# Performance work log

Measured on AMD Instinct MI355X. Metric: run time of the kernel, lower is better.

Reference implementation:

```python
import jax, jax.numpy as jnp
import numpy as np

N_NODES = 50000
N_EDGES = 800000
DIM = 128
N_LAYERS = 3
N_GRAPHS = 64
NEG_SLOPE = 0.2


def setup_inputs() -> dict:
    key = jax.random.key(0)
    ks = jax.random.split(key, 9)
    x = jax.random.normal(ks[0], (N_NODES, DIM), dtype=jnp.float32)
    edge_index = jax.random.randint(ks[1], (2, N_EDGES), 0, N_NODES, dtype=jnp.int32)
    batch = jnp.sort(jax.random.randint(ks[2], (N_NODES,), 0, N_GRAPHS, dtype=jnp.int32))
    Ws = jax.random.normal(ks[3], (N_LAYERS, DIM, DIM), dtype=jnp.float32) / np.sqrt(DIM)
    att_src = jax.random.normal(ks[4], (N_LAYERS, DIM), dtype=jnp.float32) * 0.1
    att_dst = jax.random.normal(ks[5], (N_LAYERS, DIM), dtype=jnp.float32) * 0.1
    biases = jnp.zeros((N_LAYERS, DIM), dtype=jnp.float32)
    Wf = jax.random.normal(ks[6], (DIM, 1), dtype=jnp.float32) / np.sqrt(DIM)
    bf = jnp.zeros((1,), dtype=jnp.float32)
    return {"x": x, "edge_index": edge_index, "batch": batch, "Ws": Ws,
            "att_src": att_src, "att_dst": att_dst, "biases": biases,
            "Wf": Wf, "bf": bf}


def _gat_layer(x, src, dst, W, a_src, a_dst, b, n_nodes):
    # PyG GATConv, heads=1: linear transform, per-edge attention, softmax over
    # edges incoming to each dst node, scatter-add aggregation, bias.
    h = x @ W                                        # [N, H]
    alpha = jax.nn.leaky_relu(
        (h * a_src).sum(-1)[src] + (h * a_dst).sum(-1)[dst], NEG_SLOPE)  # [E]
    m = jax.ops.segment_max(alpha, dst, num_segments=n_nodes)
    e = jnp.exp(alpha - m[dst])
    s = jax.ops.segment_sum(e, dst, num_segments=n_nodes)
    w = e / (s[dst] + 1e-16)                         # softmax per dst-neighborhood
    out = jax.ops.segment_sum(w[:, None] * h[src], dst, num_segments=n_nodes)
    return out + b


def reference(x, edge_index, batch, Ws, att_src, att_dst, biases, Wf, bf):
    n_nodes = x.shape[0]
    loop = jnp.arange(n_nodes, dtype=edge_index.dtype)   # add_self_loops=True
    src = jnp.concatenate([edge_index[0], loop])
    dst = jnp.concatenate([edge_index[1], loop])
    for l in range(N_LAYERS):
        x = _gat_layer(x, src, dst, Ws[l], att_src[l], att_dst[l], biases[l], n_nodes)
        x = jax.nn.relu(x)
    pooled = jax.ops.segment_sum(x, batch, num_segments=N_GRAPHS)  # global_add_pool
    y = (pooled @ Wf + bf).squeeze(-1)               # [N_GRAPHS]
    return y
```

## Files before the change

kernel.cpp:

```cpp
#include <hip/hip_runtime.h>
#include <hip/hip_bf16.h>

#define N_NODES 50000
#define DIM 128
#define N_GRAPHS 64
#define E_RAW 800000
#define E_TOT 850000
#define E_CAP 1200000
#define NEG_SLOPE 0.2f

typedef unsigned int uint;
typedef unsigned short ushort;
typedef float v2f __attribute__((ext_vector_type(2)));
typedef short bf16x8 __attribute__((ext_vector_type(8)));
typedef float f32x4 __attribute__((ext_vector_type(4)));

__device__ __forceinline__ int pi_pos(int p) {
    return (p >> 3) + 32 * ((p >> 1) & 3) + 16 * (p & 1);
}

__device__ __forceinline__ ushort f2bf(float f) {
    uint u = __float_as_uint(f);
    u += 0x7fffu + ((u >> 16) & 1u);
    return (ushort)(u >> 16);
}

__global__ void init_kernel(int* deg, int* fillc, float* pooled) {
    int i = blockIdx.x * blockDim.x + threadIdx.x;
    if (i < N_NODES) { deg[i] = 0; fillc[i] = 0; }
    if (i < N_GRAPHS * DIM) pooled[i] = 0.f;
}

__global__ void x2bf_kernel(const float* __restrict__ x, ushort* __restrict__ xb) {
    int i = blockIdx.x * blockDim.x + threadIdx.x;
    if (i >= N_NODES * DIM / 4) return;
    float4 v = ((const float4*)x)[i];
    ushort4 o;
    o.x = f2bf(v.x); o.y = f2bf(v.y); o.z = f2bf(v.z); o.w = f2bf(v.w);
    ((ushort4*)xb)[i] = o;
}

__global__ void wprep_kernel(const float* __restrict__ Ws, ushort* __restrict__ Wfrag) {
    int t = blockIdx.x * blockDim.x + threadIdx.x;
    if (t >= 3 * 32 * 64) return;
    int l = t >> 11;
    int rem = t & 2047;
    int chunk = rem >> 6, lane = rem & 63;
    int ks = chunk >> 3, nt = chunk & 7;
    int cc = lane & 15, gg = lane >> 4;
    const float* W = Ws + (size_t)l * DIM * DIM;
    ushort o[8];
#pragma unroll
    for (int j = 0; j < 8; ++j) {
        int kp = ks * 32 + gg * 8 + j;
        int kl = (l == 0) ? kp : pi_pos(kp);
        o[j] = f2bf(W[kl * DIM + nt * 16 + cc]);
    }
#pragma unroll
    for (int j = 0; j < 8; ++j) Wfrag[(size_t)t * 8 + j] = o[j];
}

__global__ void count_kernel(const int* __restrict__ ei, int* __restrict__ deg) {
    int e = blockIdx.x * blockDim.x + threadIdx.x;
    if (e >= E_TOT) return;
    int dst = (e < E_RAW) ? ei[E_RAW + e] : (e - E_RAW);
    atomicAdd(&deg[dst], 1);
}

__global__ void scan1_kernel(const int* __restrict__ deg, int* __restrict__ excl,
                             int* __restrict__ blksum, int n) {
    __shared__ int lds[256];
    int t = threadIdx.x;
    int i = blockIdx.x * 256 + t;
    int v = (i < n) ? ((deg[i] + 3) & ~3) : 0;
    lds[t] = v;
    __syncthreads();
    int incl = v;
    for (int off = 1; off < 256; off <<= 1) {
        int y = (t >= off) ? lds[t - off] : 0;
        __syncthreads();
        incl += y;
        lds[t] = incl;
        __syncthreads();
    }
    if (i < n) excl[i] = incl - v;
    if (t == 255) blksum[blockIdx.x] = incl;
}

__global__ void scan2_kernel(int* __restrict__ blksum, int* __restrict__ row_ptr, int nblk) {
    __shared__ int lds[256];
    int t = threadIdx.x;
    int v = (t < nblk) ? blksum[t] : 0;
    lds[t] = v;
    __syncthreads();
    int incl = v;
    for (int off = 1; off < 256; off <<= 1) {
        int y = (t >= off) ? lds[t - off] : 0;
        __syncthreads();
        incl += y;
        lds[t] = incl;
        __syncthreads();
    }
    if (t < nblk) blksum[t] = incl - v;
    if (t == nblk - 1) row_ptr[N_NODES] = incl;
}

__global__ void scan3_kernel(int* __restrict__ row_ptr, const int* __restrict__ blksum, int n) {
    int i = blockIdx.x * blockDim.x + threadIdx.x;
    if (i < n) row_ptr[i] += blksum[i >> 8];
}

__global__ void pad_kernel(const int* __restrict__ deg, const int* __restrict__ row_ptr,
                           int* __restrict__ csr_src) {
    int i = blockIdx.x * blockDim.x + threadIdx.x;
    if (i >= N_NODES) return;
    int d = deg[i];
    int pd = (d + 3) & ~3;
    int base = row_ptr[i];
    for (int k = d; k < pd; ++k) csr_src[base + k] = -1;
}

__global__ void fill_kernel(const int* __restrict__ ei, const int* __restrict__ row_ptr,
                            int* __restrict__ fillc, int* __restrict__ csr_src) {
    int e = blockIdx.x * blockDim.x + threadIdx.x;
    if (e >= E_TOT) return;
    int src, dst;
    if (e < E_RAW) { src = ei[e]; dst = ei[E_RAW + e]; }
    else           { src = dst = e - E_RAW; }
    int slot = row_ptr[dst] + atomicAdd(&fillc[dst], 1);
    csr_src[slot] = src;
}

__global__ __launch_bounds__(256) void gemm_mfma_kernel(
    const ushort* __restrict__ Xb, const ushort* __restrict__ Wfrag,
    const float* __restrict__ asrc, const float* __restrict__ adst,
    uint* __restrict__ Hb, float* __restrict__ s1, float* __restrict__ s2, int nrows) {
    int wv = threadIdx.x >> 6;
    int lane = threadIdx.x & 63;
    int c = lane & 15, g = lane >> 4;
    int row0 = blockIdx.x * 64 + wv * 16;

    int arow = row0 + c;
    if (arow >= nrows) arow = nrows - 1;
    const ushort* xrow = Xb + (size_t)arow * DIM;

    f32x4 acc[8];
#pragma unroll
    for (int nt = 0; nt < 8; ++nt) acc[nt] = (f32x4)(0.f);

#pragma unroll
    for (int ks = 0; ks < 4; ++ks) {
        bf16x8 afrag = *(const bf16x8*)(xrow + ks * 32 + g * 8);
#pragma unroll
        for (int nt = 0; nt < 8; ++nt) {
            bf16x8 bfrag = *(const bf16x8*)(Wfrag + ((size_t)(ks * 8 + nt) * 64 + lane) * 8);
            acc[nt] = __builtin_amdgcn_mfma_f32_16x16x32_bf16(afrag, bfrag, acc[nt], 0, 0, 0);
        }
    }

    float a1[8], a2[8];
#pragma unroll
    for (int nt = 0; nt < 8; ++nt) { a1[nt] = asrc[c + 16 * nt]; a2[nt] = adst[c + 16 * nt]; }

#pragma unroll
    for (int r = 0; r < 4; ++r) {
        int outrow = row0 + g * 4 + r;
        bool valid = outrow < nrows;
        if (valid) {
            int w0 = __builtin_amdgcn_cvt_pk_fp8_f32(acc[0][r], acc[1][r], 0, false);
            w0     = __builtin_amdgcn_cvt_pk_fp8_f32(acc[2][r], acc[3][r], w0, true);
            int w1 = __builtin_amdgcn_cvt_pk_fp8_f32(acc[4][r], acc[5][r], 0, false);
            w1     = __builtin_amdgcn_cvt_pk_fp8_f32(acc[6][r], acc[7][r], w1, true);
            *(uint2*)&Hb[(size_t)outrow * 32 + c * 2] = make_uint2((uint)w0, (uint)w1);
        }
        float p1 = 0.f, p2 = 0.f;
#pragma unroll
        for (int nt = 0; nt < 8; ++nt) {
            p1 = fmaf(acc[nt][r], a1[nt], p1);
            p2 = fmaf(acc[nt][r], a2[nt], p2);
        }
#pragma unroll
        for (int m = 1; m < 16; m <<= 1) { p1 += __shfl_xor(p1, m); p2 += __shfl_xor(p2, m); }
        if (c == 0 && valid) { s1[outrow] = p1; s2[outrow] = p2; }
    }
}

__global__ __launch_bounds__(256) void agg_kernel(
    const ushort* __restrict__ Hb16, const int* __restrict__ csr_src,
    const int* __restrict__ row_ptr, const float* __restrict__ s1,
    const float* __restrict__ s2n, const float* __restrict__ bias,
    ushort* __restrict__ Xout, const int* __restrict__ batch,
    float* __restrict__ pooled, int pool_flag, int ngroups) {
    int gw = (blockIdx.x * blockDim.x + threadIdx.x) >> 6;
    int lane = threadIdx.x & 63;
    if (gw >= ngroups) return;
    int node0 = gw * 8;

    int4 rpa = *(const int4*)&row_ptr[node0];
    int4 rpb = *(const int4*)&row_ptr[node0 + 4];
    int rp8 = row_ptr[node0 + 8];
    int rp[9] = {rpa.x, rpa.y, rpa.z, rpa.w, rpb.x, rpb.y, rpb.z, rpb.w, rp8};
    float4 s2qa = *(const float4*)&s2n[node0];
    float4 s2qb = *(const float4*)&s2n[node0 + 4];
    float s2a[8] = {s2qa.x, s2qa.y, s2qa.z, s2qa.w, s2qb.x, s2qb.y, s2qb.z, s2qb.w};
    int cc = lane >> 2, ii = lane & 3;
    float2 b2;
    b2.x = bias[cc + 32 * ii];
    b2.y = bias[cc + 32 * ii + 16];
    int ba[8] = {0, 0, 0, 0, 0, 0, 0, 0};
    if (pool_flag) {
        int4 bqa = *(const int4*)&batch[node0];
        int4 bqb = *(const int4*)&batch[node0 + 4];
        ba[0] = bqa.x; ba[1] = bqa.y; ba[2] = bqa.z; ba[3] = bqa.w;
        ba[4] = bqb.x; ba[5] = bqb.y; ba[6] = bqb.z; ba[7] = bqb.w;
    }

#pragma unroll
    for (int k = 0; k < 8; ++k) {
        int beg = rp[k], end = rp[k + 1];
        float s2v = s2a[k];
        float2 acc = make_float2(0.f, 0.f);
        float wsum = 0.f;

        for (int s = beg; s < end; s += 8) {
            int4 a = *(const int4*)&csr_src[s];
            bool vb = (s + 4) < end;
            int4 b = vb ? *(const int4*)&csr_src[s + 4] : make_int4(-1, -1, -1, -1);
            int sn[8] = {a.x, a.y, a.z, a.w, b.x, b.y, b.z, b.w};
            ushort hv[8];
#pragma unroll
            for (int j = 0; j < 8; ++j) {
                int r = (sn[j] < 0) ? 0 : sn[j];
                hv[j] = Hb16[(size_t)r * 64 + lane];
            }
            float w[8];
#pragma unroll
            for (int j = 0; j < 8; ++j) {
                int r = (sn[j] < 0) ? 0 : sn[j];
                float al = s1[r] + s2v;
                al = (al > 0.f) ? al : NEG_SLOPE * al;
                float e = __expf(al);
                w[j] = (sn[j] < 0) ? 0.f : e;
                wsum += w[j];
            }
#pragma unroll
            for (int j = 0; j < 8; ++j) {
                v2f f = __builtin_amdgcn_cvt_pk_f32_fp8((int)hv[j], false);
                acc.x = fmaf(w[j], f.x, acc.x);
                acc.y = fmaf(w[j], f.y, acc.y);
            }
        }

        float inv = 1.f / (wsum + 1e-16f);
        acc.x = fmaxf(fmaf(acc.x, inv, b2.x), 0.f);
        acc.y = fmaxf(fmaf(acc.y, inv, b2.y), 0.f);
        if (pool_flag) {
            atomicAdd(&pooled[ba[k] * DIM + 2 * lane], acc.x);
            atomicAdd(&pooled[ba[k] * DIM + 2 * lane + 1], acc.y);
        } else {
            ushort2 hb;
            hb.x = f2bf(acc.x);
            hb.y = f2bf(acc.y);
            ((ushort2*)Xout)[(size_t)(node0 + k) * 64 + lane] = hb;
        }
    }
}

__global__ void final_kernel(const float* __restrict__ pooled, const float* __restrict__ Wf,
                             const float* __restrict__ bf, float* __restrict__ y) {
    int wid = (blockIdx.x * blockDim.x + threadIdx.x) >> 6;
    int lane = threadIdx.x & 63;
    if (wid >= N_GRAPHS) return;
    float2 p = *(const float2*)&pooled[wid * DIM + 2 * lane];
    int cc = lane >> 2, ii = lane & 3;
    float wx = Wf[cc + 32 * ii];
    float wy = Wf[cc + 32 * ii + 16];
    float v = p.x * wx + p.y * wy;
    for (int off = 32; off; off >>= 1) v += __shfl_down(v, off);
    if (lane == 0) y[wid] = v + bf[0];
}

extern "C" void kernel_launch(void* const* d_in, const int* in_sizes, int n_in,
                              void* d_out, int out_size, void* d_ws, size_t ws_size,
                              hipStream_t stream) {
    const float* x       = (const float*)d_in[0];
    const int*   ei      = (const int*)d_in[1];
    const int*   batch   = (const int*)d_in[2];
    const float* Ws      = (const float*)d_in[3];
    const float* att_src = (const float*)d_in[4];
    const float* att_dst = (const float*)d_in[5];
    const float* biases  = (const float*)d_in[6];
    const float* Wf      = (const float*)d_in[7];
    const float* bf      = (const float*)d_in[8];
    float* y = (float*)d_out;

    char* p = (char*)d_ws;
    auto alloc = [&](size_t bytes) -> void* {
        void* r = (void*)p;
        p += (bytes + 255) & ~(size_t)255;
        return r;
    };
    ushort* xC     = (ushort*)alloc((size_t)(N_NODES + 64) * DIM * 2);
    ushort* xA     = (ushort*)alloc((size_t)(N_NODES + 64) * DIM * 2);
    uint*   Hb     = (uint*)alloc((size_t)N_NODES * 32 * 4);
    ushort* Wfrag  = (ushort*)alloc((size_t)3 * 32 * 64 * 8 * 2);
    int*   csr_src = (int*)alloc((size_t)E_CAP * 4);
    int*   deg     = (int*)alloc((size_t)N_NODES * 4);
    int*   fillc   = (int*)alloc((size_t)N_NODES * 4);
    int*   row_ptr = (int*)alloc((size_t)(N_NODES + 16) * 4);
    int*   blksum  = (int*)alloc(256 * 4);
    float* s1      = (float*)alloc((size_t)N_NODES * 4);
    float* s2      = (float*)alloc((size_t)(N_NODES + 8) * 4);
    float* pooled  = (float*)alloc((size_t)N_GRAPHS * DIM * 4);

    const int BN = 256;
    const int gN   = (N_NODES + BN - 1) / BN;
    const int gE   = (E_TOT + BN - 1) / BN;
    const int ngroups = N_NODES / 8;
    const int gAGG = (ngroups * 64 + BN - 1) / BN;
    const int nblk = gN;
    const int gCVT = (N_NODES * DIM / 4 + BN - 1) / BN;
    const int gGEMM = (N_NODES + 63) / 64;

    init_kernel<<<gN, BN, 0, stream>>>(deg, fillc, pooled);
    x2bf_kernel<<<gCVT, BN, 0, stream>>>(x, xC);
    wprep_kernel<<<(3 * 32 * 64 + BN - 1) / BN, BN, 0, stream>>>(Ws, Wfrag);
    count_kernel<<<gE, BN, 0, stream>>>(ei, deg);
    scan1_kernel<<<nblk, BN, 0, stream>>>(deg, row_ptr, blksum, N_NODES);
    scan2_kernel<<<1, BN, 0, stream>>>(blksum, row_ptr, nblk);
    scan3_kernel<<<gN, BN, 0, stream>>>(row_ptr, blksum, N_NODES);
    pad_kernel<<<gN, BN, 0, stream>>>(deg, row_ptr, csr_src);
    fill_kernel<<<gE, BN, 0, stream>>>(ei, row_ptr, fillc, csr_src);

    const ushort* xin = xC;
    ushort* xout = xA;
    for (int l = 0; l < 3; ++l) {
        const ushort* Wf_l = Wfrag + (size_t)l * 32 * 64 * 8;
        const float* as = att_src + (size_t)l * DIM;
        const float* ad = att_dst + (size_t)l * DIM;
        const float* b  = biases + (size_t)l * DIM;

        gemm_mfma_kernel<<<gGEMM, BN, 0, stream>>>(xin, Wf_l, as, ad, Hb, s1, s2, N_NODES);
        agg_kernel<<<gAGG, BN, 0, stream>>>((const ushort*)Hb, csr_src, row_ptr, s1, s2, b,
                                            xout, batch, pooled,
                                            (l == 2) ? 1 : 0, ngroups);
        xin = xout;
        xout = (l == 0) ? xC : xA;
    }

    final_kernel<<<(N_GRAPHS * 64 + BN - 1) / BN, BN, 0, stream>>>(pooled, Wf, bf, y);
    (void)ws_size; (void)n_in; (void)in_sizes; (void)out_size;
}
```

Baseline: 378.1 us.

## Precompute per-edge attention weights in a separate kernel and split gather across half-waves

Adds an ew_kernel that computes the leaky-relu/exp attention weight for every CSR slot once per layer, using a new csr_dst array written during fill. The aggregation kernel then loads precomputed weights instead of gathering s1 and evaluating exp redundantly in all 64 lanes. Each half-wave now gathers a different neighbour as a 4-byte fp8 word and the halves are combined with a shuffle. Padding is replaced by pre-filling csr_src with -1 over a fixed slot count. The cost is an extra kernel launch and extra weight and dst traffic each layer, and correctness depends on padded slots staying within NSLOT.

```diff
diff --git a/kernel.cpp b/kernel.cpp
--- a/kernel.cpp
+++ b/kernel.cpp
@@ -6,6 +6,7 @@
 #define N_GRAPHS 64
 #define E_RAW 800000
 #define E_TOT 850000
+#define NSLOT 1000000
 #define E_CAP 1200000
 #define NEG_SLOPE 0.2f
 
@@ -29,6 +30,11 @@
     int i = blockIdx.x * blockDim.x + threadIdx.x;
     if (i < N_NODES) { deg[i] = 0; fillc[i] = 0; }
     if (i < N_GRAPHS * DIM) pooled[i] = 0.f;
+}
+
+__global__ void csr_init_kernel(int* __restrict__ csr_src) {
+    int i = blockIdx.x * blockDim.x + threadIdx.x;
+    if (i < NSLOT / 4) ((int4*)csr_src)[i] = make_int4(-1, -1, -1, -1);
 }
 
 __global__ void x2bf_kernel(const float* __restrict__ x, ushort* __restrict__ xb) {
@@ -110,18 +116,9 @@
     if (i < n) row_ptr[i] += blksum[i >> 8];
 }
 
-__global__ void pad_kernel(const int* __restrict__ deg, const int* __restrict__ row_ptr,
-                           int* __restrict__ csr_src) {
-    int i = blockIdx.x * blockDim.x + threadIdx.x;
-    if (i >= N_NODES) return;
-    int d = deg[i];
-    int pd = (d + 3) & ~3;
-    int base = row_ptr[i];
-    for (int k = d; k < pd; ++k) csr_src[base + k] = -1;
-}
-
 __global__ void fill_kernel(const int* __restrict__ ei, const int* __restrict__ row_ptr,
-                            int* __restrict__ fillc, int* __restrict__ csr_src) {
+                            int* __restrict__ fillc, int* __restrict__ csr_src,
+                            int* __restrict__ csr_dst) {
     int e = blockIdx.x * blockDim.x + threadIdx.x;
     if (e >= E_TOT) return;
     int src, dst;
@@ -129,6 +126,7 @@
     else           { src = dst = e - E_RAW; }
     int slot = row_ptr[dst] + atomicAdd(&fillc[dst], 1);
     csr_src[slot] = src;
+    csr_dst[slot] = dst;
 }
 
 __global__ __launch_bounds__(256) void gemm_mfma_kernel(
@@ -185,28 +183,46 @@
     }
 }
 
+__global__ __launch_bounds__(256) void ew_kernel(
+    const int* __restrict__ csr_src, const int* __restrict__ csr_dst,
+    const float* __restrict__ s1, const float* __restrict__ s2,
+    float* __restrict__ w) {
+    int slot = blockIdx.x * blockDim.x + threadIdx.x;
+    if (slot >= NSLOT) return;
+    int sv = csr_src[slot];
+    float wv = 0.f;
+    if (sv >= 0) {
+        int dv = csr_dst[slot];
+        float al = s1[sv] + s2[dv];
+        al = fmaxf(al, NEG_SLOPE * al);
+        wv = __expf(al);
+    }
+    w[slot] = wv;
+}
+
 __global__ __launch_bounds__(256) void agg_kernel(
-    const ushort* __restrict__ Hb16, const int* __restrict__ csr_src,
-    const int* __restrict__ row_ptr, const float* __restrict__ s1,
-    const float* __restrict__ s2n, const float* __restrict__ bias,
+    const uint* __restrict__ Hb, const int* __restrict__ csr_src,
+    const int* __restrict__ row_ptr, const float* __restrict__ w,
+    const float* __restrict__ bias,
     ushort* __restrict__ Xout, const int* __restrict__ batch,
     float* __restrict__ pooled, int pool_flag, int ngroups) {
     int gw = (blockIdx.x * blockDim.x + threadIdx.x) >> 6;
     int lane = threadIdx.x & 63;
     if (gw >= ngroups) return;
     int node0 = gw * 8;
+    int q = lane & 31;
+    int h = lane >> 5;
 
     int4 rpa = *(const int4*)&row_ptr[node0];
     int4 rpb = *(const int4*)&row_ptr[node0 + 4];
     int rp8 = row_ptr[node0 + 8];
     int rp[9] = {rpa.x, rpa.y, rpa.z, rpa.w, rpb.x, rpb.y, rpb.z, rpb.w, rp8};
-    float4 s2qa = *(const float4*)&s2n[node0];
-    float4 s2qb = *(const float4*)&s2n[node0 + 4];
-    float s2a[8] = {s2qa.x, s2qa.y, s2qa.z, s2qa.w, s2qb.x, s2qb.y, s2qb.z, s2qb.w};
-    int cc = lane >> 2, ii = lane & 3;
+
+    int p0 = 4 * q + 2 * h;
     float2 b2;
-    b2.x = bias[cc + 32 * ii];
-    b2.y = bias[cc + 32 * ii + 16];
+    b2.x = bias[pi_pos(p0)];
+    b2.y = bias[pi_pos(p0) + 16];
+
     int ba[8] = {0, 0, 0, 0, 0, 0, 0, 0};
     if (pool_flag) {
         int4 bqa = *(const int4*)&batch[node0];
@@ -218,50 +234,52 @@
 #pragma unroll
     for (int k = 0; k < 8; ++k) {
         int beg = rp[k], end = rp[k + 1];
-        float s2v = s2a[k];
-        float2 acc = make_float2(0.f, 0.f);
-        float wsum = 0.f;
+        float acc0 = 0.f, acc1 = 0.f, acc2 = 0.f, acc3 = 0.f, ws = 0.f;
 
         for (int s = beg; s < end; s += 8) {
             int4 a = *(const int4*)&csr_src[s];
+            float4 wa = *(const float4*)&w[s];
             bool vb = (s + 4) < end;
             int4 b = vb ? *(const int4*)&csr_src[s + 4] : make_int4(-1, -1, -1, -1);
+            float4 wb = vb ? *(const float4*)&w[s + 4] : make_float4(0.f, 0.f, 0.f, 0.f);
             int sn[8] = {a.x, a.y, a.z, a.w, b.x, b.y, b.z, b.w};
-            ushort hv[8];
-#pragma unroll
-            for (int j = 0; j < 8; ++j) {
-                int r = (sn[j] < 0) ? 0 : sn[j];
-                hv[j] = Hb16[(size_t)r * 64 + lane];
+            float wv[8] = {wa.x, wa.y, wa.z, wa.w, wb.x, wb.y, wb.z, wb.w};
+#pragma unroll
+            for (int p2 = 0; p2 < 4; ++p2) {
+                int r0 = sn[2 * p2];     r0 = (r0 < 0) ? 0 : r0;
+                int r1 = sn[2 * p2 + 1]; r1 = (r1 < 0) ? 0 : r1;
+                int rsel = h ? r1 : r0;
+                float wsel = h ? wv[2 * p2 + 1] : wv[2 * p2];
+                uint hv = Hb[(size_t)rsel * 32 + q];
+                v2f f0 = __builtin_amdgcn_cvt_pk_f32_fp8((int)hv, false);
+                v2f f1 = __builtin_amdgcn_cvt_pk_f32_fp8((int)hv, true);
+                acc0 = fmaf(wsel, f0.x, acc0);
+                acc1 = fmaf(wsel, f0.y, acc1);
+                acc2 = fmaf(wsel, f1.x, acc2);
+                acc3 = fmaf(wsel, f1.y, acc3);
+                ws += wsel;
             }
-            float w[8];
-#pragma unroll
-            for (int j = 0; j < 8; ++j) {
-                int r = (sn[j] < 0) ? 0 : sn[j];
-                float al = s1[r] + s2v;
-                al = (al > 0.f) ? al : NEG_SLOPE * al;
-                float e = __expf(al);
-                w[j] = (sn[j] < 0) ? 0.f : e;
-                wsum += w[j];
-            }
-#pragma unroll
-            for (int j = 0; j < 8; ++j) {
-                v2f f = __builtin_amdgcn_cvt_pk_f32_fp8((int)hv[j], false);
-                acc.x = fmaf(w[j], f.x, acc.x);
-                acc.y = fmaf(w[j], f.y, acc.y);
-            }
-        }
-
-        float inv = 1.f / (wsum + 1e-16f);
-        acc.x = fmaxf(fmaf(acc.x, inv, b2.x), 0.f);
-        acc.y = fmaxf(fmaf(acc.y, inv, b2.y), 0.f);
+        }
+
+        acc0 += __shfl_xor(acc0, 32);
+        acc1 += __shfl_xor(acc1, 32);
+        acc2 += __shfl_xor(acc2, 32);
+        acc3 += __shfl_xor(acc3, 32);
+        ws   += __shfl_xor(ws, 32);
+        float inv = 1.f / (ws + 1e-16f);
+        float vx = h ? acc2 : acc0;
+        float vy = h ? acc3 : acc1;
+        vx = fmaxf(fmaf(vx, inv, b2.x), 0.f);
+        vy = fmaxf(fmaf(vy, inv, b2.y), 0.f);
+
         if (pool_flag) {
-            atomicAdd(&pooled[ba[k] * DIM + 2 * lane], acc.x);
-            atomicAdd(&pooled[ba[k] * DIM + 2 * lane + 1], acc.y);
+            atomicAdd(&pooled[ba[k] * DIM + p0], vx);
+            atomicAdd(&pooled[ba[k] * DIM + p0 + 1], vy);
         } else {
             ushort2 hb;
-            hb.x = f2bf(acc.x);
-            hb.y = f2bf(acc.y);
-            ((ushort2*)Xout)[(size_t)(node0 + k) * 64 + lane] = hb;
+            hb.x = f2bf(vx);
+            hb.y = f2bf(vy);
+            ((ushort2*)Xout)[(size_t)(node0 + k) * 64 + (p0 >> 1)] = hb;
         }
     }
 }
@@ -305,6 +323,8 @@
     uint*   Hb     = (uint*)alloc((size_t)N_NODES * 32 * 4);
     ushort* Wfrag  = (ushort*)alloc((size_t)3 * 32 * 64 * 8 * 2);
     int*   csr_src = (int*)alloc((size_t)E_CAP * 4);
+    int*   csr_dst = (int*)alloc((size_t)E_CAP * 4);
+    float* wbuf    = (float*)alloc((size_t)E_CAP * 4);
     int*   deg     = (int*)alloc((size_t)N_NODES * 4);
     int*   fillc   = (int*)alloc((size_t)N_NODES * 4);
     int*   row_ptr = (int*)alloc((size_t)(N_NODES + 16) * 4);
@@ -321,16 +341,18 @@
     const int nblk = gN;
     const int gCVT = (N_NODES * DIM / 4 + BN - 1) / BN;
     const int gGEMM = (N_NODES + 63) / 64;
+    const int gEW  = (NSLOT + BN - 1) / BN;
+    const int gCI  = (NSLOT / 4 + BN - 1) / BN;
 
     init_kernel<<<gN, BN, 0, stream>>>(deg, fillc, pooled);
+    csr_init_kernel<<<gCI, BN, 0, stream>>>(csr_src);
     x2bf_kernel<<<gCVT, BN, 0, stream>>>(x, xC);
     wprep_kernel<<<(3 * 32 * 64 + BN - 1) / BN, BN, 0, stream>>>(Ws, Wfrag);
     count_kernel<<<gE, BN, 0, stream>>>(ei, deg);
     scan1_kernel<<<nblk, BN, 0, stream>>>(deg, row_ptr, blksum, N_NODES);
     scan2_kernel<<<1, BN, 0, stream>>>(blksum, row_ptr, nblk);
     scan3_kernel<<<gN, BN, 0, stream>>>(row_ptr, blksum, N_NODES);
-    pad_kernel<<<gN, BN, 0, stream>>>(deg, row_ptr, csr_src);
-    fill_kernel<<<gE, BN, 0, stream>>>(ei, row_ptr, fillc, csr_src);
+    fill_kernel<<<gE, BN, 0, stream>>>(ei, row_ptr, fillc, csr_src, csr_dst);
 
     const ushort* xin = xC;
     ushort* xout = xA;
@@ -341,7 +363,8 @@
         const float* b  = biases + (size_t)l * DIM;
 
         gemm_mfma_kernel<<<gGEMM, BN, 0, stream>>>(xin, Wf_l, as, ad, Hb, s1, s2, N_NODES);
-        agg_kernel<<<gAGG, BN, 0, stream>>>((const ushort*)Hb, csr_src, row_ptr, s1, s2, b,
+        ew_kernel<<<gEW, BN, 0, stream>>>(csr_src, csr_dst, s1, s2, wbuf);
+        agg_kernel<<<gAGG, BN, 0, stream>>>(Hb, csr_src, row_ptr, wbuf, b,
                                             xout, batch, pooled,
                                             (l == 2) ? 1 : 0, ngroups);
         xin = xout;
```

Measured after the change: 379.2 us. Within noise of the previous version (+0.3%).
